# Kernel optimization log

Measured on AMD Instinct MI355X. Metric: run time of the kernel, lower is better.

## Reference

```python
import jax, jax.numpy as jnp
import numpy as np

B, S, H = 2, 2048, 1024
NH, NKV, HD = 16, 16, 64
R, KF = 16, 4
THETA = 1000000.0


def setup_inputs() -> dict:
    key = jax.random.key(0)
    ks = jax.random.split(key, 16)
    sc = 0.02
    signs = jax.random.randint(ks[13], (1, 1, 1, KF, HD // 2), 0, 2).astype(jnp.float32) * 2 - 1
    cdma = jnp.concatenate([signs, signs], axis=-1)  # [1,1,1,KF,HD]
    return {
        "hidden_states": jax.random.normal(ks[0], (B, S, H), jnp.float32),
        "position_ids": jnp.broadcast_to(jnp.arange(S, dtype=jnp.int32), (B, S)),
        "q_w": jax.random.normal(ks[1], (H, H), jnp.float32) * sc,
        "q_b": jax.random.normal(ks[2], (H,), jnp.float32) * sc,
        "k_w": jax.random.normal(ks[3], (H, H), jnp.float32) * sc,
        "k_b": jax.random.normal(ks[4], (H,), jnp.float32) * sc,
        "v_w": jax.random.normal(ks[5], (H, H), jnp.float32) * sc,
        "v_b": jax.random.normal(ks[6], (H,), jnp.float32) * sc,
        "o_w": jax.random.normal(ks[7], (H, H), jnp.float32) * sc,
        "lora_qA": jax.random.normal(ks[8], (R, H), jnp.float32) * sc,
        "lora_qB": jax.random.normal(ks[9], (H, R), jnp.float32) * sc,
        "lora_vA": jax.random.normal(ks[10], (R, H), jnp.float32) * sc,
        "lora_vB": jax.random.normal(ks[11], (H, R), jnp.float32) * sc,
        "cdma_keys": cdma,
    }


def _rope(q, k, position_ids):
    # cos/sin per HF rotary embedding, theta=1e6 (Qwen1.5)
    inv_freq = 1.0 / (THETA ** (jnp.arange(0, HD, 2, dtype=jnp.float32) / HD))  # [HD/2]
    freqs = position_ids.astype(jnp.float32)[..., None] * inv_freq  # [B,S,HD/2]
    emb = jnp.concatenate([freqs, freqs], axis=-1)  # [B,S,HD]
    cos = jnp.cos(emb)[:, None]  # [B,1,S,HD]
    sin = jnp.sin(emb)[:, None]

    def rot_half(x):
        return jnp.concatenate([-x[..., HD // 2:], x[..., :HD // 2]], axis=-1)

    return q * cos + rot_half(q) * sin, k * cos + rot_half(k) * sin


def reference(hidden_states, position_ids, q_w, q_b, k_w, k_b, v_w, v_b, o_w,
              lora_qA, lora_qB, lora_vA, lora_vB, cdma_keys):
    bsz, q_len, _ = hidden_states.shape
    # base projections + LoRA adjustments (k has no LoRA)
    q = hidden_states @ q_w.T + q_b + (hidden_states @ lora_qA.T) @ lora_qB.T
    k = hidden_states @ k_w.T + k_b
    v = hidden_states @ v_w.T + v_b + (hidden_states @ lora_vA.T) @ lora_vB.T

    q = q.reshape(bsz, q_len, NH, HD).transpose(0, 2, 1, 3)   # [B,NH,S,HD]
    k = k.reshape(bsz, q_len, NKV, HD).transpose(0, 2, 1, 3)  # [B,NKV,S,HD]
    v = v.reshape(bsz, q_len, NKV, HD).transpose(0, 2, 1, 3)

    q, k = _rope(q, k, position_ids)

    # holographic block sign-bind/sum transform (q_len divisible by KF -> no pad)
    n_slots = q_len // KF
    k_blocks = k.reshape(bsz, NKV, n_slots, KF, HD)
    v_blocks = v.reshape(bsz, NKV, n_slots, KF, HD)
    S_K = jnp.sum(k_blocks * cdma_keys, axis=3, keepdims=True)  # [B,NKV,slots,1,HD]
    S_V = jnp.sum(v_blocks * cdma_keys, axis=3, keepdims=True)
    K_noisy = (S_K * cdma_keys).reshape(bsz, NKV, q_len, HD)
    V_noisy = (S_V * cdma_keys).reshape(bsz, NKV, q_len, HD)

    scale = 1.0 / (np.sqrt(HD) * np.sqrt(KF))
    scores = jnp.einsum('bhqd,bhkd->bhqk', q, K_noisy) * scale
    causal = jnp.tril(jnp.ones((q_len, q_len), dtype=bool))
    scores = jnp.where(causal, scores, jnp.float32(-1e9))
    attn = jax.nn.softmax(scores, axis=-1)
    out = jnp.einsum('bhqk,bhkd->bhqd', attn, V_noisy)
    out = out.transpose(0, 2, 1, 3).reshape(bsz, q_len, NH * HD)
    return out @ o_w.T
```

## Files before the change

### kernel.cpp

```cpp
#include <hip/hip_runtime.h>
#include <hip/hip_bf16.h>
#include <math.h>


typedef __bf16 bf16;
typedef __attribute__((ext_vector_type(8))) __bf16 bf16x8;
typedef __attribute__((ext_vector_type(4))) float f32x4;
typedef __attribute__((ext_vector_type(2))) unsigned u32x2;

#define NB 2
#define SEQ 2048
#define HID 1024
#define NHD 16
#define HDD 64

__device__ __forceinline__ void gld_lds16(const void* g, void* l) {
  __builtin_amdgcn_global_load_lds(
      (const __attribute__((address_space(1))) void*)g,
      (__attribute__((address_space(3))) void*)l, 16, 0, 0);
}

__device__ __forceinline__ unsigned pack2bf(float a, float b) {
  unsigned short ua = __builtin_bit_cast(unsigned short, (bf16)a);
  unsigned short ub = __builtin_bit_cast(unsigned short, (bf16)b);
  return ((unsigned)ub << 16) | ua;
}

#define PB_W    3072
#define PB_HS   (PB_W + 4096)
#define PB_OW   (PB_HS + 1024)
#define PB_BIAS (PB_OW + 12)
#define PB_TAB  (PB_BIAS + 256)

__global__ __launch_bounds__(256) void prep_all(
    const float* __restrict__ hs, const float* __restrict__ ow,
    const float* __restrict__ qw, const float* __restrict__ qb,
    const float* __restrict__ kw, const float* __restrict__ kb,
    const float* __restrict__ vw, const float* __restrict__ vb,
    const float* __restrict__ qA, const float* __restrict__ qB,
    const float* __restrict__ vA, const float* __restrict__ vB,
    bf16* __restrict__ hsb, bf16* __restrict__ owb, bf16* __restrict__ Wqkv,
    float* __restrict__ bqkv, float* __restrict__ ct, float* __restrict__ st) {
  const int bid = blockIdx.x, tid = threadIdx.x;
  if (bid < PB_W) {
    int idx = bid * 256 + tid;
    int n = idx >> 8, k4 = (idx & 255) << 2;
    f32x4 v;
    if (n < 1024) {
      v = *(const f32x4*)(qw + (size_t)n * 1024 + k4);
#pragma unroll
      for (int r = 0; r < 16; ++r) {
        float bq = qB[n * 16 + r];
        f32x4 a = *(const f32x4*)(qA + (size_t)r * 1024 + k4);
        v.x += bq * a.x; v.y += bq * a.y; v.z += bq * a.z; v.w += bq * a.w;
      }
    } else if (n < 2048) {
      v = *(const f32x4*)(kw + (size_t)(n - 1024) * 1024 + k4);
    } else {
      int nn = n - 2048;
      v = *(const f32x4*)(vw + (size_t)nn * 1024 + k4);
#pragma unroll
      for (int r = 0; r < 16; ++r) {
        float bv = vB[nn * 16 + r];
        f32x4 a = *(const f32x4*)(vA + (size_t)r * 1024 + k4);
        v.x += bv * a.x; v.y += bv * a.y; v.z += bv * a.z; v.w += bv * a.w;
      }
    }
    int seg = k4 >> 6, cl = k4 & 63;
    int ch = (cl >> 3) ^ (n & 7);
    u32x2 u; u.x = pack2bf(v.x, v.y); u.y = pack2bf(v.z, v.w);
    *(u32x2*)(Wqkv + (size_t)n * 1024 + (seg << 6) + (ch << 3) + (cl & 7)) = u;
  } else if (bid < PB_HS) {
    int idx = (bid - PB_W) * 256 + tid;
    int r = idx >> 8, c4 = (idx & 255) << 2;
    f32x4 v = *(const f32x4*)(hs + (size_t)r * 1024 + c4);
    int seg = c4 >> 6, cl = c4 & 63;
    int ch = (cl >> 3) ^ (r & 7);
    u32x2 u; u.x = pack2bf(v.x, v.y); u.y = pack2bf(v.z, v.w);
    *(u32x2*)(hsb + (size_t)r * 1024 + (seg << 6) + (ch << 3) + (cl & 7)) = u;
  } else if (bid < PB_OW) {
    int idx = (bid - PB_HS) * 256 + tid;
    int r = idx >> 8, c4 = (idx & 255) << 2;
    f32x4 v = *(const f32x4*)(ow + (size_t)r * 1024 + c4);
    int seg = c4 >> 6, cl = c4 & 63;
    int ch = (cl >> 3) ^ (r & 7);
    u32x2 u; u.x = pack2bf(v.x, v.y); u.y = pack2bf(v.z, v.w);
    *(u32x2*)(owb + (size_t)r * 1024 + (seg << 6) + (ch << 3) + (cl & 7)) = u;
  } else if (bid < PB_BIAS) {
    int i = (bid - PB_OW) * 256 + tid;
    if (i < 3072)
      bqkv[i] = (i < 1024) ? qb[i] : (i < 2048 ? kb[i - 1024] : vb[i - 2048]);
  } else {
    int idx = (bid - PB_BIAS) * 256 + tid;
    int s = idx >> 5, i = idx & 31;
    double inv = pow(1.0e6, -(double)i / 32.0);
    double a = (double)s * inv;
    ct[idx] = (float)cos(a);
    st[idx] = (float)sin(a);
  }
}

__global__ __launch_bounds__(256, 4) void gemm_bt(
    const bf16* __restrict__ A, const bf16* __restrict__ Bw,
    const float* __restrict__ bias, bf16* __restrict__ Cb,
    float* __restrict__ Cf, int M, int N, int K) {
  __shared__ __align__(16) bf16 As[128 * 64];
  __shared__ __align__(16) bf16 Bs[128 * 64];
  const int tid = threadIdx.x;
  const int lane = tid & 63, w = tid >> 6;
  const int wm = w >> 1, wn = w & 1;
  const int l15 = lane & 15, l4 = lane >> 4;
  const int m0 = blockIdx.y * 128, n0 = blockIdx.x * 128;
  const size_t rowb = (size_t)K * 2;
  const char* gA = (const char*)A + (size_t)m0 * rowb;
  const char* gB = (const char*)Bw + (size_t)n0 * rowb;
  f32x4 acc[4][4] = {};

  for (int k0 = 0; k0 < K; k0 += 64) {
    const char* gAk = gA + k0 * 2;
    const char* gBk = gB + k0 * 2;
#pragma unroll
    for (int i = 0; i < 4; ++i) {
      int idx = i * 256 + tid;
      int row = idx >> 3, ch = idx & 7;
      gld_lds16(gAk + (size_t)row * rowb + ch * 16,
                (char*)As + (i * 256 + (w << 6)) * 16);
      gld_lds16(gBk + (size_t)row * rowb + ch * 16,
                (char*)Bs + (i * 256 + (w << 6)) * 16);
    }
    __syncthreads();
#pragma unroll
    for (int c = 0; c < 2; ++c) {
      bf16x8 af[4], bfr[4];
#pragma unroll
      for (int mi = 0; mi < 4; ++mi) {
        int row = wm * 64 + mi * 16 + l15;
        int ch = (c * 4 + l4) ^ (row & 7);
        af[mi] = *(const bf16x8*)(As + row * 64 + ch * 8);
      }
#pragma unroll
      for (int ni = 0; ni < 4; ++ni) {
        int row = wn * 64 + ni * 16 + l15;
        int ch = (c * 4 + l4) ^ (row & 7);
        bfr[ni] = *(const bf16x8*)(Bs + row * 64 + ch * 8);
      }
#pragma unroll
      for (int mi = 0; mi < 4; ++mi)
#pragma unroll
        for (int ni = 0; ni < 4; ++ni)
          acc[mi][ni] = __builtin_amdgcn_mfma_f32_16x16x32_bf16(
              af[mi], bfr[ni], acc[mi][ni], 0, 0, 0);
    }
    __syncthreads();
  }
#pragma unroll
  for (int mi = 0; mi < 4; ++mi) {
    int rbase = m0 + wm * 64 + mi * 16 + l4 * 4;
#pragma unroll
    for (int ni = 0; ni < 4; ++ni) {
      int col = n0 + wn * 64 + ni * 16 + l15;
      float badd = bias ? bias[col] : 0.0f;
#pragma unroll
      for (int r = 0; r < 4; ++r) {
        float v = acc[mi][ni][r] + badd;
        if (Cf) Cf[(size_t)(rbase + r) * N + col] = v;
        else    Cb[(size_t)(rbase + r) * N + col] = (bf16)v;
      }
    }
  }
}

__global__ __launch_bounds__(256) void rope_holo(
    const bf16* __restrict__ qkv, const int* __restrict__ pos,
    const float* __restrict__ ct, const float* __restrict__ st,
    const float* __restrict__ cdma, bf16* __restrict__ Qr,
    bf16* __restrict__ Kn, bf16* __restrict__ Vt) {
  const int bid = blockIdx.x, tid = threadIdx.x;
  if (bid < 1024) {
    const float SCQ = 0.0901684403f;
    int idx = bid * 256 + tid;
    int ih = idx & 3, s = (idx >> 2) & 2047, h = (idx >> 13) & 15, b = idx >> 17;
    int p = pos[b * SEQ + s];
    size_t base = ((size_t)(b * SEQ + s)) * 3072 + h * 64 + ih * 8;
    bf16x8 xv = *(const bf16x8*)(qkv + base);
    bf16x8 yv = *(const bf16x8*)(qkv + base + 32);
    const float* ctp = ct + p * 32 + ih * 8;
    const float* stp = st + p * 32 + ih * 8;
    bf16x8 o0, o1;
#pragma unroll
    for (int e = 0; e < 8; ++e) {
      float x = (float)xv[e], y = (float)yv[e];
      float co = ctp[e], sn = stp[e];
      o0[e] = (bf16)((x * co - y * sn) * SCQ);
      o1[e] = (bf16)((y * co + x * sn) * SCQ);
    }
    size_t ob = ((size_t)((b * 16 + h) * SEQ + s)) * 64 + ih * 8;
    *(bf16x8*)(Qr + ob) = o0;
    *(bf16x8*)(Qr + ob + 32) = o1;
  } else {
    int idx = (bid - 1024) * 256 + tid;
    int ih = idx & 3, slot = (idx >> 2) & 511, h = (idx >> 11) & 15, b = idx >> 15;
    float SK[8] = {}, SK2[8] = {}, SV[8] = {}, SV2[8] = {};
#pragma unroll
    for (int f = 0; f < 4; ++f) {
      int s = slot * 4 + f;
      size_t base = ((size_t)(b * SEQ + s)) * 3072 + h * 64 + ih * 8;
      bf16x8 klo = *(const bf16x8*)(qkv + base + 1024);
      bf16x8 khi = *(const bf16x8*)(qkv + base + 1024 + 32);
      bf16x8 vlo = *(const bf16x8*)(qkv + base + 2048);
      bf16x8 vhi = *(const bf16x8*)(qkv + base + 2048 + 32);
      int p = pos[b * SEQ + s];
      const float* ctp = ct + p * 32 + ih * 8;
      const float* stp = st + p * 32 + ih * 8;
      const float* cdp = cdma + f * 64 + ih * 8;
#pragma unroll
      for (int e = 0; e < 8; ++e) {
        float cf = cdp[e];
        float kx = (float)klo[e], ky = (float)khi[e];
        float co = ctp[e], sn = stp[e];
        SK[e]  += (kx * co - ky * sn) * cf;
        SK2[e] += (ky * co + kx * sn) * cf;
        SV[e]  += (float)vlo[e] * cf;
        SV2[e] += (float)vhi[e] * cf;
      }
    }
    size_t hb = (size_t)(b * 16 + h);
#pragma unroll
    for (int f = 0; f < 4; ++f) {
      int s = slot * 4 + f;
      const float* cdp = cdma + f * 64 + ih * 8;
      bf16x8 k0, k1;
#pragma unroll
      for (int e = 0; e < 8; ++e) {
        k0[e] = (bf16)(SK[e] * cdp[e]);
        k1[e] = (bf16)(SK2[e] * cdp[e]);
      }
      size_t krow = (hb * SEQ + s) * 64;
      int ch0 = ih ^ (s & 7);
      int ch1 = (4 + ih) ^ (s & 7);
      *(bf16x8*)(Kn + krow + ch0 * 8) = k0;
      *(bf16x8*)(Kn + krow + ch1 * 8) = k1;
      int seg = s >> 6, cl = s & 63;
      size_t vcol = (size_t)(seg << 6) + (cl & 7);
#pragma unroll
      for (int e = 0; e < 8; ++e) {
        int i = ih * 8 + e;
        int vch = (cl >> 3) ^ (i & 7);
        Vt[(hb * 64 + i) * (size_t)SEQ + vcol + vch * 8] = (bf16)(SV[e] * cdp[e]);
        Vt[(hb * 64 + i + 32) * (size_t)SEQ + vcol + vch * 8] = (bf16)(SV2[e] * cdp[e]);
      }
    }
  }
}

__global__ __launch_bounds__(256) void attn_fwd(
    const bf16* __restrict__ Qr, const bf16* __restrict__ Kn,
    const bf16* __restrict__ Vt, bf16* __restrict__ AO) {
  __shared__ __align__(16) bf16 Kt[2][128 * 64];
  __shared__ __align__(16) bf16 Vl[2][64 * 128];
  __shared__ __align__(16) bf16 Pt[4][16 * 128];
  const int L = ((blockIdx.x & 7) << 6) + (blockIdx.x >> 3);
  const int pq = L & 15, h = (L >> 4) & 15, b = L >> 8;
  const int tid = threadIdx.x, lane = tid & 63, w = tid >> 6;
  const int l15 = lane & 15, l4 = lane >> 4;
  const size_t hd = ((size_t)(b * 16 + h)) * SEQ * 64;
  const char* gK0 = (const char*)(Kn + hd);
  const char* gV0 = (const char*)(Vt + hd);
  char* pw = (char*)&Pt[w][0];

#pragma unroll 1
  for (int phase = 0; phase < 2; ++phase) {
    const int qt = phase ? (31 - pq) : pq;
    const int q0 = qt * 64;
    const int qg = q0 + w * 16 + l15;
    const int nt = (qt >> 1) + 1;

    const bf16* qb = Qr + hd + (size_t)qg * 64;
    bf16x8 qf0 = *(const bf16x8*)(qb + l4 * 8);
    bf16x8 qf1 = *(const bf16x8*)(qb + 32 + l4 * 8);

    f32x4 oacc[4] = {};
    float m = -1e30f, lsum = 0.0f;

#pragma unroll
    for (int i = 0; i < 4; ++i)
      gld_lds16(gK0 + (i * 256 + tid) * 16,
                (char*)Kt[0] + (i * 256 + (w << 6)) * 16);
#pragma unroll
    for (int i = 0; i < 4; ++i) {
      int idx = i * 256 + tid;
      int row = idx >> 4, ch = idx & 15;
      gld_lds16(gV0 + (size_t)row * (SEQ * 2) + ch * 16,
                (char*)Vl[0] + (i * 256 + (w << 6)) * 16);
    }

#pragma unroll 1
    for (int t = 0; t < nt; ++t) {
      const int cur = t & 1;
      if (t + 1 < nt) {
        const int tn = t + 1, sb = cur ^ 1;
#pragma unroll
        for (int i = 0; i < 4; ++i)
          gld_lds16(gK0 + (size_t)tn * 16384 + (i * 256 + tid) * 16,
                    (char*)Kt[sb] + (i * 256 + (w << 6)) * 16);
#pragma unroll
        for (int i = 0; i < 4; ++i) {
          int idx = i * 256 + tid;
          int row = idx >> 4, ch = idx & 15;
          gld_lds16(gV0 + (size_t)row * (SEQ * 2) + tn * 256 + ch * 16,
                    (char*)Vl[sb] + (i * 256 + (w << 6)) * 16);
        }
        asm volatile("s_waitcnt vmcnt(8)\ns_barrier" ::: "memory");
      } else {
        asm volatile("s_waitcnt vmcnt(0)\ns_barrier" ::: "memory");
      }

      const bf16* Ktc = Kt[cur];
      const bf16* Vlc = Vl[cur];
      const int kv0 = t * 128;
      const bool lastt = (t == nt - 1);

      f32x4 sacc[8] = {};
#pragma unroll
      for (int c = 0; c < 2; ++c) {
        bf16x8 qf = c ? qf1 : qf0;
#pragma unroll
        for (int nf = 0; nf < 8; ++nf) {
          int row = nf * 16 + l15;
          int ch = (c * 4 + l4) ^ (row & 7);
          bf16x8 kf = *(const bf16x8*)(Ktc + row * 64 + ch * 8);
          sacc[nf] = __builtin_amdgcn_mfma_f32_16x16x32_bf16(kf, qf, sacc[nf], 0, 0, 0);
        }
      }

      float px[4] = {-1e30f, -1e30f, -1e30f, -1e30f};
      if (lastt) {
#pragma unroll
        for (int nf = 0; nf < 8; ++nf)
#pragma unroll
          for (int r = 0; r < 4; ++r) {
            int kvg = kv0 + nf * 16 + l4 * 4 + r;
            float v = (kvg > qg) ? -1e30f : sacc[nf][r];
            sacc[nf][r] = v;
            px[nf & 3] = fmaxf(px[nf & 3], v);
          }
      } else {
#pragma unroll
        for (int nf = 0; nf < 8; ++nf)
#pragma unroll
          for (int r = 0; r < 4; ++r) px[nf & 3] = fmaxf(px[nf & 3], sacc[nf][r]);
      }
      float pmax = fmaxf(fmaxf(px[0], px[1]), fmaxf(px[2], px[3]));
      pmax = fmaxf(pmax, __shfl_xor(pmax, 16));
      pmax = fmaxf(pmax, __shfl_xor(pmax, 32));

      if (!__all(pmax <= m)) {
        float mn = fmaxf(m, pmax);
        float al = exp2f(m - mn);
        m = mn;
        lsum *= al;
#pragma unroll
        for (int df = 0; df < 4; ++df) oacc[df] *= al;
      }
      float rs4[4] = {0.f, 0.f, 0.f, 0.f};
#pragma unroll
      for (int nf = 0; nf < 8; ++nf)
#pragma unroll
        for (int r = 0; r < 4; ++r) {
          float e = exp2f(sacc[nf][r] - m);
          sacc[nf][r] = e;
          rs4[nf & 3] += e;
        }
      float rs = (rs4[0] + rs4[1]) + (rs4[2] + rs4[3]);
      rs += __shfl_xor(rs, 16);
      rs += __shfl_xor(rs, 32);
      lsum += rs;

#pragma unroll
      for (int nf = 0; nf < 8; ++nf) {
        u32x2 u;
        u.x = pack2bf(sacc[nf][0], sacc[nf][1]);
        u.y = pack2bf(sacc[nf][2], sacc[nf][3]);
        int boff = (l15 * 256 + nf * 32 + l4 * 8) ^ ((l15 & 7) << 4);
        *(u32x2*)(pw + boff) = u;
      }

#pragma unroll
      for (int c2 = 0; c2 < 4; ++c2) {
        int pb = (l15 * 256 + c2 * 64 + l4 * 16) ^ ((l15 & 7) << 4);
        bf16x8 pf = *(const bf16x8*)(pw + pb);
        int vbyte = (c2 * 64 + l4 * 16) ^ ((l15 & 7) << 4);
#pragma unroll
        for (int df = 0; df < 4; ++df) {
          int vrow = df * 16 + l15;
          bf16x8 vf = *(const bf16x8*)((const char*)Vlc + vrow * 256 + vbyte);
          oacc[df] = __builtin_amdgcn_mfma_f32_16x16x32_bf16(vf, pf, oacc[df], 0, 0, 0);
        }
      }
      asm volatile("s_barrier" ::: "memory");
    }

    const float li = 1.0f / lsum;
    const size_t arow = ((size_t)(b * SEQ + qg)) * HID + h * 64;
    const int qk7 = qg & 7;
#pragma unroll
    for (int df = 0; df < 4; ++df) {
      int ch = (df * 2 + (l4 >> 1)) ^ qk7;
      u32x2 u;
      u.x = pack2bf(oacc[df][0] * li, oacc[df][1] * li);
      u.y = pack2bf(oacc[df][2] * li, oacc[df][3] * li);
      *(u32x2*)(AO + arow + ch * 8 + (l4 & 1) * 4) = u;
    }
  }
}

extern "C" void kernel_launch(void* const* d_in, const int* in_sizes, int n_in,
                              void* d_out, int out_size, void* d_ws, size_t ws_size,
                              hipStream_t stream) {
  const float* hs  = (const float*)d_in[0];
  const int* pos   = (const int*)d_in[1];
  const float* qw  = (const float*)d_in[2];
  const float* qb_ = (const float*)d_in[3];
  const float* kw  = (const float*)d_in[4];
  const float* kb_ = (const float*)d_in[5];
  const float* vw  = (const float*)d_in[6];
  const float* vb_ = (const float*)d_in[7];
  const float* ow  = (const float*)d_in[8];
  const float* qA  = (const float*)d_in[9];
  const float* qB  = (const float*)d_in[10];
  const float* vA  = (const float*)d_in[11];
  const float* vB  = (const float*)d_in[12];
  const float* cd  = (const float*)d_in[13];

  char* p = (char*)d_ws;
  auto alloc = [&](size_t bytes) {
    char* r = p; p += (bytes + 255) & ~(size_t)255; return r;
  };
  bf16* hsb   = (bf16*)alloc((size_t)4096 * 1024 * 2);
  bf16* Wqkv  = (bf16*)alloc((size_t)3072 * 1024 * 2);
  float* bqkv = (float*)alloc(3072 * 4);
  bf16* owb   = (bf16*)alloc((size_t)1024 * 1024 * 2);
  bf16* qkvb  = (bf16*)alloc((size_t)4096 * 3072 * 2);
  float* ct   = (float*)alloc((size_t)SEQ * 32 * 4);
  float* st   = (float*)alloc((size_t)SEQ * 32 * 4);
  bf16* Qrb   = (bf16*)alloc((size_t)NB * NHD * SEQ * 64 * 2);
  bf16* Knb   = (bf16*)alloc((size_t)NB * NHD * SEQ * 64 * 2);
  bf16* Vtb   = (bf16*)alloc((size_t)NB * NHD * 64 * SEQ * 2);
  bf16* AOb   = (bf16*)alloc((size_t)4096 * 1024 * 2);

  prep_all<<<dim3(PB_TAB), 256, 0, stream>>>(
      hs, ow, qw, qb_, kw, kb_, vw, vb_, qA, qB, vA, vB,
      hsb, owb, Wqkv, bqkv, ct, st);
  gemm_bt<<<dim3(3072 / 128, 4096 / 128), 256, 0, stream>>>(
      hsb, Wqkv, bqkv, qkvb, nullptr, 4096, 3072, 1024);
  rope_holo<<<dim3(1024 + 256), 256, 0, stream>>>(
      qkvb, pos, ct, st, cd, Qrb, Knb, Vtb);
  attn_fwd<<<dim3(512), 256, 0, stream>>>(Qrb, Knb, Vtb, AOb);
  gemm_bt<<<dim3(1024 / 128, 4096 / 128), 256, 0, stream>>>(
      AOb, owb, nullptr, nullptr, (float*)d_out, 4096, 1024, 1024);
}
```

Baseline: 148.2 us.

## Split attention into one q-tile per block, load V directly to registers

The attention kernel no longer pairs two query tiles per block. It now launches 1024 blocks, each handling one 64-row query tile, ordered heaviest-first (qt descending) so causal load imbalance is absorbed by scheduling. The V tile no longer goes through LDS: each lane loads its swizzled V fragments straight from global memory into registers each iteration, which drops the V LDS buffer and halves the async-copy wait count. This cuts LDS use and may raise occupancy, but V loads become synchronous global loads on the critical path and raise register pressure.

```diff
diff --git a/kernel.cpp b/kernel.cpp
--- a/kernel.cpp
+++ b/kernel.cpp
@@ -257,160 +257,163 @@
     const bf16* __restrict__ Qr, const bf16* __restrict__ Kn,
     const bf16* __restrict__ Vt, bf16* __restrict__ AO) {
   __shared__ __align__(16) bf16 Kt[2][128 * 64];
-  __shared__ __align__(16) bf16 Vl[2][64 * 128];
   __shared__ __align__(16) bf16 Pt[4][16 * 128];
-  const int L = ((blockIdx.x & 7) << 6) + (blockIdx.x >> 3);
-  const int pq = L & 15, h = (L >> 4) & 15, b = L >> 8;
+  const int bid = blockIdx.x;
+  const int t8 = bid >> 3;
+  const int qt = 31 - (t8 >> 2);
+  const int hb = (bid & 7) * 4 + (t8 & 3);
+  const int h = hb & 15, b = hb >> 4;
   const int tid = threadIdx.x, lane = tid & 63, w = tid >> 6;
   const int l15 = lane & 15, l4 = lane >> 4;
+  const int q0 = qt * 64;
+  const int qg = q0 + w * 16 + l15;
+  const int nt = (qt >> 1) + 1;
   const size_t hd = ((size_t)(b * 16 + h)) * SEQ * 64;
   const char* gK0 = (const char*)(Kn + hd);
   const char* gV0 = (const char*)(Vt + hd);
   char* pw = (char*)&Pt[w][0];
+  const int vswz = (l15 & 7) << 4;
+
+  const bf16* qb = Qr + hd + (size_t)qg * 64;
+  bf16x8 qf0 = *(const bf16x8*)(qb + l4 * 8);
+  bf16x8 qf1 = *(const bf16x8*)(qb + 32 + l4 * 8);
+
+  f32x4 oacc[4] = {};
+  float m = -1e30f, lsum = 0.0f;
+
+#pragma unroll
+  for (int i = 0; i < 4; ++i)
+    gld_lds16(gK0 + (i * 256 + tid) * 16,
+              (char*)Kt[0] + (i * 256 + (w << 6)) * 16);
 
 #pragma unroll 1
-  for (int phase = 0; phase < 2; ++phase) {
-    const int qt = phase ? (31 - pq) : pq;
-    const int q0 = qt * 64;
-    const int qg = q0 + w * 16 + l15;
-    const int nt = (qt >> 1) + 1;
-
-    const bf16* qb = Qr + hd + (size_t)qg * 64;
-    bf16x8 qf0 = *(const bf16x8*)(qb + l4 * 8);
-    bf16x8 qf1 = *(const bf16x8*)(qb + 32 + l4 * 8);
-
-    f32x4 oacc[4] = {};
-    float m = -1e30f, lsum = 0.0f;
-
-#pragma unroll
-    for (int i = 0; i < 4; ++i)
-      gld_lds16(gK0 + (i * 256 + tid) * 16,
-                (char*)Kt[0] + (i * 256 + (w << 6)) * 16);
-#pragma unroll
-    for (int i = 0; i < 4; ++i) {
-      int idx = i * 256 + tid;
-      int row = idx >> 4, ch = idx & 15;
-      gld_lds16(gV0 + (size_t)row * (SEQ * 2) + ch * 16,
-                (char*)Vl[0] + (i * 256 + (w << 6)) * 16);
-    }
-
-#pragma unroll 1
-    for (int t = 0; t < nt; ++t) {
-      const int cur = t & 1;
-      if (t + 1 < nt) {
-        const int tn = t + 1, sb = cur ^ 1;
-#pragma unroll
-        for (int i = 0; i < 4; ++i)
-          gld_lds16(gK0 + (size_t)tn * 16384 + (i * 256 + tid) * 16,
-                    (char*)Kt[sb] + (i * 256 + (w << 6)) * 16);
-#pragma unroll
-        for (int i = 0; i < 4; ++i) {
-          int idx = i * 256 + tid;
-          int row = idx >> 4, ch = idx & 15;
-          gld_lds16(gV0 + (size_t)row * (SEQ * 2) + tn * 256 + ch * 16,
-                    (char*)Vl[sb] + (i * 256 + (w << 6)) * 16);
+  for (int t = 0; t < nt; ++t) {
+    const int cur = t & 1;
+    if (t + 1 < nt) {
+#pragma unroll
+      for (int i = 0; i < 4; ++i)
+        gld_lds16(gK0 + (size_t)(t + 1) * 16384 + (i * 256 + tid) * 16,
+                  (char*)Kt[cur ^ 1] + (i * 256 + (w << 6)) * 16);
+      asm volatile("s_waitcnt vmcnt(4)\ns_barrier" ::: "memory");
+    } else {
+      asm volatile("s_waitcnt vmcnt(0)\ns_barrier" ::: "memory");
+    }
+
+    const bf16* Ktc = Kt[cur];
+    const int kv0 = t * 128;
+    const bool lastt = (t == nt - 1);
+
+    f32x4 sacc[8] = {};
+#pragma unroll
+    for (int c = 0; c < 2; ++c) {
+      bf16x8 qf = c ? qf1 : qf0;
+#pragma unroll
+      for (int nf = 0; nf < 8; ++nf) {
+        int row = nf * 16 + l15;
+        int ch = (c * 4 + l4) ^ (row & 7);
+        bf16x8 kf = *(const bf16x8*)(Ktc + row * 64 + ch * 8);
+        sacc[nf] = __builtin_amdgcn_mfma_f32_16x16x32_bf16(kf, qf, sacc[nf], 0, 0, 0);
+      }
+    }
+
+    const char* gVt = gV0 + (size_t)kv0 * 2;
+    bf16x8 va[4], vb[4], vc[4], vd[4];
+#pragma unroll
+    for (int df = 0; df < 4; ++df) {
+      const char* rb = gVt + (size_t)(df * 16 + l15) * (SEQ * 2);
+      va[df] = *(const bf16x8*)(rb + ((0 * 64 + l4 * 16) ^ vswz));
+      vb[df] = *(const bf16x8*)(rb + ((1 * 64 + l4 * 16) ^ vswz));
+      vc[df] = *(const bf16x8*)(rb + ((2 * 64 + l4 * 16) ^ vswz));
+      vd[df] = *(const bf16x8*)(rb + ((3 * 64 + l4 * 16) ^ vswz));
+    }
+
+    float px[4] = {-1e30f, -1e30f, -1e30f, -1e30f};
+    if (lastt) {
+#pragma unroll
+      for (int nf = 0; nf < 8; ++nf)
+#pragma unroll
+        for (int r = 0; r < 4; ++r) {
+          int kvg = kv0 + nf * 16 + l4 * 4 + r;
+          float v = (kvg > qg) ? -1e30f : sacc[nf][r];
+          sacc[nf][r] = v;
+          px[nf & 3] = fmaxf(px[nf & 3], v);
         }
-        asm volatile("s_waitcnt vmcnt(8)\ns_barrier" ::: "memory");
-      } else {
-        asm volatile("s_waitcnt vmcnt(0)\ns_barrier" ::: "memory");
-      }
-
-      const bf16* Ktc = Kt[cur];
-      const bf16* Vlc = Vl[cur];
-      const int kv0 = t * 128;
-      const bool lastt = (t == nt - 1);
-
-      f32x4 sacc[8] = {};
-#pragma unroll
-      for (int c = 0; c < 2; ++c) {
-        bf16x8 qf = c ? qf1 : qf0;
-#pragma unroll
-        for (int nf = 0; nf < 8; ++nf) {
-          int row = nf * 16 + l15;
-          int ch = (c * 4 + l4) ^ (row & 7);
-          bf16x8 kf = *(const bf16x8*)(Ktc + row * 64 + ch * 8);
-          sacc[nf] = __builtin_amdgcn_mfma_f32_16x16x32_bf16(kf, qf, sacc[nf], 0, 0, 0);
-        }
-      }
-
-      float px[4] = {-1e30f, -1e30f, -1e30f, -1e30f};
-      if (lastt) {
-#pragma unroll
-        for (int nf = 0; nf < 8; ++nf)
-#pragma unroll
-          for (int r = 0; r < 4; ++r) {
-            int kvg = kv0 + nf * 16 + l4 * 4 + r;
-            float v = (kvg > qg) ? -1e30f : sacc[nf][r];
-            sacc[nf][r] = v;
-            px[nf & 3] = fmaxf(px[nf & 3], v);
-          }
-      } else {
-#pragma unroll
-        for (int nf = 0; nf < 8; ++nf)
-#pragma unroll
-          for (int r = 0; r < 4; ++r) px[nf & 3] = fmaxf(px[nf & 3], sacc[nf][r]);
-      }
-      float pmax = fmaxf(fmaxf(px[0], px[1]), fmaxf(px[2], px[3]));
-      pmax = fmaxf(pmax, __shfl_xor(pmax, 16));
-      pmax = fmaxf(pmax, __shfl_xor(pmax, 32));
-
-      if (!__all(pmax <= m)) {
-        float mn = fmaxf(m, pmax);
-        float al = exp2f(m - mn);
-        m = mn;
-        lsum *= al;
-#pragma unroll
-        for (int df = 0; df < 4; ++df) oacc[df] *= al;
-      }
-      float rs4[4] = {0.f, 0.f, 0.f, 0.f};
+    } else {
 #pragma unroll
       for (int nf = 0; nf < 8; ++nf)
 #pragma unroll
-        for (int r = 0; r < 4; ++r) {
-          float e = exp2f(sacc[nf][r] - m);
-          sacc[nf][r] = e;
-          rs4[nf & 3] += e;
-        }
-      float rs = (rs4[0] + rs4[1]) + (rs4[2] + rs4[3]);
-      rs += __shfl_xor(rs, 16);
-      rs += __shfl_xor(rs, 32);
-      lsum += rs;
-
-#pragma unroll
-      for (int nf = 0; nf < 8; ++nf) {
-        u32x2 u;
-        u.x = pack2bf(sacc[nf][0], sacc[nf][1]);
-        u.y = pack2bf(sacc[nf][2], sacc[nf][3]);
-        int boff = (l15 * 256 + nf * 32 + l4 * 8) ^ ((l15 & 7) << 4);
-        *(u32x2*)(pw + boff) = u;
-      }
-
-#pragma unroll
-      for (int c2 = 0; c2 < 4; ++c2) {
-        int pb = (l15 * 256 + c2 * 64 + l4 * 16) ^ ((l15 & 7) << 4);
-        bf16x8 pf = *(const bf16x8*)(pw + pb);
-        int vbyte = (c2 * 64 + l4 * 16) ^ ((l15 & 7) << 4);
-#pragma unroll
-        for (int df = 0; df < 4; ++df) {
-          int vrow = df * 16 + l15;
-          bf16x8 vf = *(const bf16x8*)((const char*)Vlc + vrow * 256 + vbyte);
-          oacc[df] = __builtin_amdgcn_mfma_f32_16x16x32_bf16(vf, pf, oacc[df], 0, 0, 0);
-        }
-      }
-      asm volatile("s_barrier" ::: "memory");
-    }
-
-    const float li = 1.0f / lsum;
-    const size_t arow = ((size_t)(b * SEQ + qg)) * HID + h * 64;
-    const int qk7 = qg & 7;
-#pragma unroll
-    for (int df = 0; df < 4; ++df) {
-      int ch = (df * 2 + (l4 >> 1)) ^ qk7;
+        for (int r = 0; r < 4; ++r) px[nf & 3] = fmaxf(px[nf & 3], sacc[nf][r]);
+    }
+    float pmax = fmaxf(fmaxf(px[0], px[1]), fmaxf(px[2], px[3]));
+    pmax = fmaxf(pmax, __shfl_xor(pmax, 16));
+    pmax = fmaxf(pmax, __shfl_xor(pmax, 32));
+
+    if (!__all(pmax <= m)) {
+      float mn = fmaxf(m, pmax);
+      float al = exp2f(m - mn);
+      m = mn;
+      lsum *= al;
+#pragma unroll
+      for (int df = 0; df < 4; ++df) oacc[df] *= al;
+    }
+    float rs4[4] = {0.f, 0.f, 0.f, 0.f};
+#pragma unroll
+    for (int nf = 0; nf < 8; ++nf)
+#pragma unroll
+      for (int r = 0; r < 4; ++r) {
+        float e = exp2f(sacc[nf][r] - m);
+        sacc[nf][r] = e;
+        rs4[nf & 3] += e;
+      }
+    float rs = (rs4[0] + rs4[1]) + (rs4[2] + rs4[3]);
+    rs += __shfl_xor(rs, 16);
+    rs += __shfl_xor(rs, 32);
+    lsum += rs;
+
+#pragma unroll
+    for (int nf = 0; nf < 8; ++nf) {
       u32x2 u;
-      u.x = pack2bf(oacc[df][0] * li, oacc[df][1] * li);
-      u.y = pack2bf(oacc[df][2] * li, oacc[df][3] * li);
-      *(u32x2*)(AO + arow + ch * 8 + (l4 & 1) * 4) = u;
-    }
+      u.x = pack2bf(sacc[nf][0], sacc[nf][1]);
+      u.y = pack2bf(sacc[nf][2], sacc[nf][3]);
+      int boff = (l15 * 256 + nf * 32 + l4 * 8) ^ vswz;
+      *(u32x2*)(pw + boff) = u;
+    }
+
+    {
+      int pb0 = (l15 * 256 + 0 * 64 + l4 * 16) ^ vswz;
+      bf16x8 pf = *(const bf16x8*)(pw + pb0);
+#pragma unroll
+      for (int df = 0; df < 4; ++df)
+        oacc[df] = __builtin_amdgcn_mfma_f32_16x16x32_bf16(va[df], pf, oacc[df], 0, 0, 0);
+      int pb1 = (l15 * 256 + 1 * 64 + l4 * 16) ^ vswz;
+      pf = *(const bf16x8*)(pw + pb1);
+#pragma unroll
+      for (int df = 0; df < 4; ++df)
+        oacc[df] = __builtin_amdgcn_mfma_f32_16x16x32_bf16(vb[df], pf, oacc[df], 0, 0, 0);
+      int pb2 = (l15 * 256 + 2 * 64 + l4 * 16) ^ vswz;
+      pf = *(const bf16x8*)(pw + pb2);
+#pragma unroll
+      for (int df = 0; df < 4; ++df)
+        oacc[df] = __builtin_amdgcn_mfma_f32_16x16x32_bf16(vc[df], pf, oacc[df], 0, 0, 0);
+      int pb3 = (l15 * 256 + 3 * 64 + l4 * 16) ^ vswz;
+      pf = *(const bf16x8*)(pw + pb3);
+#pragma unroll
+      for (int df = 0; df < 4; ++df)
+        oacc[df] = __builtin_amdgcn_mfma_f32_16x16x32_bf16(vd[df], pf, oacc[df], 0, 0, 0);
+    }
+    asm volatile("s_barrier" ::: "memory");
+  }
+
+  const float li = 1.0f / lsum;
+  const size_t arow = ((size_t)(b * SEQ + qg)) * HID + h * 64;
+  const int qk7 = qg & 7;
+#pragma unroll
+  for (int df = 0; df < 4; ++df) {
+    int ch = (df * 2 + (l4 >> 1)) ^ qk7;
+    u32x2 u;
+    u.x = pack2bf(oacc[df][0] * li, oacc[df][1] * li);
+    u.y = pack2bf(oacc[df][2] * li, oacc[df][3] * li);
+    *(u32x2*)(AO + arow + ch * 8 + (l4 & 1) * 4) = u;
   }
 }
 
@@ -455,7 +458,7 @@
       hsb, Wqkv, bqkv, qkvb, nullptr, 4096, 3072, 1024);
   rope_holo<<<dim3(1024 + 256), 256, 0, stream>>>(
       qkvb, pos, ct, st, cd, Qrb, Knb, Vtb);
-  attn_fwd<<<dim3(512), 256, 0, stream>>>(Qrb, Knb, Vtb, AOb);
+  attn_fwd<<<dim3(1024), 256, 0, stream>>>(Qrb, Knb, Vtb, AOb);
   gemm_bt<<<dim3(1024 / 128, 4096 / 128), 256, 0, stream>>>(
       AOb, owb, nullptr, nullptr, (float*)d_out, 4096, 1024, 1024);
 }
```

Measured after the change: 162.7 us. 1.1x slower.
